# Kernel optimization log

Hardware: AMD Instinct MI355X
Metric: run time of the kernel (lower is better)

## Reference

```python
import jax, jax.numpy as jnp
import numpy as np

B, H, W = 64, 256, 256
G = 64
V = G * G          # 4096
HID = 512
S = 50


def _conv(x, w, b):
    # x: (B,C,H,W), w: (O,I,3,3) -> 'same' conv, NCHW
    y = jax.lax.conv_general_dilated(x, w, (1, 1), 'SAME',
                                     dimension_numbers=('NCHW', 'OIHW', 'NCHW'))
    return y + b[None, :, None, None]


def setup_inputs() -> dict:
    key = jax.random.key(0)
    ks = jax.random.split(key, 14)

    def lin(k, shape, fan_in):
        return (jax.random.normal(k, shape, jnp.float32) / np.float32(np.sqrt(fan_in)))

    return {
        'mask': jax.random.uniform(ks[0], (B, 1, H, W), jnp.float32),
        'target_ids': jax.random.randint(ks[1], (B, S), 0, V),
        'conv1_w': lin(ks[2], (16, 1, 3, 3), 9), 'conv1_b': jnp.zeros((16,), jnp.float32),
        'conv2_w': lin(ks[3], (32, 16, 3, 3), 16 * 9), 'conv2_b': jnp.zeros((32,), jnp.float32),
        'feat_w': lin(ks[4], (HID, 32), 32), 'feat_b': jnp.zeros((HID,), jnp.float32),
        'ctx_w': lin(ks[5], (HID, HID), HID), 'ctx_b': jnp.zeros((HID,), jnp.float32),
        'tok_emb': jax.random.normal(ks[6], (V + 1, HID), jnp.float32) * 0.02,
        'w_ih': lin(ks[7], (4 * HID, HID), HID), 'w_hh': lin(ks[8], (4 * HID, HID), HID),
        'b_ih': jnp.zeros((4 * HID,), jnp.float32), 'b_hh': jnp.zeros((4 * HID,), jnp.float32),
        'head_w': lin(ks[9], (V, HID), HID), 'head_b': jnp.zeros((V,), jnp.float32),
    }


def reference(mask, target_ids, conv1_w, conv1_b, conv2_w, conv2_b,
              feat_w, feat_b, ctx_w, ctx_b, tok_emb,
              w_ih, w_hh, b_ih, b_hh, head_w, head_b):
    b = mask.shape[0]
    vocab = head_w.shape[0]

    # --- CNN encoder ---
    x = jax.nn.relu(_conv(mask, conv1_w, conv1_b))                    # (B,16,H,W)
    x = jax.lax.reduce_window(x, -jnp.inf, jax.lax.max,
                              (1, 1, 2, 2), (1, 1, 2, 2), 'VALID')    # (B,16,H/2,W/2)
    x = jax.nn.relu(_conv(x, conv2_w, conv2_b))                       # (B,32,H/2,W/2)
    x = x.mean(axis=(2, 3))                                           # AdaptiveAvgPool2d(1) -> (B,32)

    h0 = x @ feat_w.T + feat_b                                        # (B,HID)
    c0 = jnp.zeros_like(h0)
    ctx = h0 @ ctx_w.T + ctx_b                                        # (B,HID)

    # Full teacher forcing (ratio=1.0): input token at t=0 is start token V,
    # at t>0 it is target_ids[:, t-1]. All embeddings gathered upfront.
    start = jnp.full((b, 1), vocab, dtype=target_ids.dtype)
    toks = jnp.concatenate([start, target_ids[:, :-1]], axis=1)       # (B,S)
    embs = tok_emb[toks]                                              # (B,S,HID)
    lstm_in = jnp.swapaxes(embs, 0, 1) + ctx[None]                    # (S,B,HID)

    bias = b_ih + b_hh

    def step(carry, inp):
        h, c = carry
        gates = inp @ w_ih.T + h @ w_hh.T + bias                      # (B,4*HID)
        i, f, g, o = jnp.split(gates, 4, axis=-1)
        c = jax.nn.sigmoid(f) * c + jax.nn.sigmoid(i) * jnp.tanh(g)
        h = jax.nn.sigmoid(o) * jnp.tanh(c)
        logit = h @ head_w.T + head_b                                 # (B,V)
        return (h, c), logit

    _, logits = jax.lax.scan(step, (h0, c0), lstm_in)                 # (S,B,V)
    return jnp.swapaxes(logits, 0, 1)                                 # (B,S,V)
```

## Files before the change

### kernel.cpp

```cpp
#include <hip/hip_runtime.h>
#include <cmath>

typedef __attribute__((ext_vector_type(8))) _Float16 f16x8;
typedef __attribute__((ext_vector_type(4))) float f32x4;
typedef __attribute__((ext_vector_type(4))) unsigned u32x4;

#define LSTM_NB 32

__device__ __forceinline__ unsigned short f2h(float x) {
  return __builtin_bit_cast(unsigned short, (_Float16)x);
}

__device__ __forceinline__ void gload16(const void* g, void* l) {
  __builtin_amdgcn_global_load_lds(
      (const __attribute__((address_space(1))) void*)g,
      (__attribute__((address_space(3))) void*)l, 16, 0, 0);
}

__device__ __forceinline__ void cload16(const void* p, u32x4* dst) {
  asm volatile("global_load_dwordx4 %0, %1, off sc0 sc1"
               : "=v"(*dst)
               : "v"(p));
}

__global__ __launch_bounds__(512) void k_conv(
    const float* __restrict__ mask, const float* __restrict__ w1,
    const float* __restrict__ b1, const float* __restrict__ w2,
    const float* __restrict__ b2, float* __restrict__ part)
{
  __shared__ float s_p1[16][18 * 36];
  __shared__ float s_w1[144];
  __shared__ float s_b1[16];
  __shared__ float s_w2[4608];
  __shared__ float s_b2[32];

  const int tid = threadIdx.x;
  const int b = blockIdx.x >> 5;
  const int tile = blockIdx.x & 31;
  const int px0 = (tile & 3) * 32, py0 = (tile >> 2) * 16;
  const float* mb = mask + (size_t)b * 65536;

  for (int i = tid; i < 144; i += 512) s_w1[i] = w1[i];
  for (int i = tid; i < 4608; i += 512) s_w2[i] = w2[i];
  if (tid < 16) s_b1[tid] = b1[tid];
  if (tid < 32) s_b2[tid] = b2[tid];
  __syncthreads();

  for (int idx = tid; idx < 18 * 34; idx += 512) {
    int ly = idx / 34, lx = idx - ly * 34;
    int py = py0 - 1 + ly, px = px0 - 1 + lx;
    if (py < 0 || py >= 128 || px < 0 || px >= 128) {
      for (int o = 0; o < 16; o++) s_p1[o][ly * 36 + lx] = 0.f;
    } else {
      float patch[4][4];
      int gy0 = 2 * py - 1, gx0 = 2 * px - 1;
#pragma unroll
      for (int i = 0; i < 4; i++) {
        int gy = gy0 + i;
        bool yok = (gy >= 0 && gy < 256);
#pragma unroll
        for (int j = 0; j < 4; j++) {
          int gx = gx0 + j;
          patch[i][j] = (yok && gx >= 0 && gx < 256) ? mb[gy * 256 + gx] : 0.f;
        }
      }
      for (int o = 0; o < 16; o++) {
        float m = 0.f;
#pragma unroll
        for (int dy = 0; dy < 2; dy++)
#pragma unroll
          for (int dx = 0; dx < 2; dx++) {
            float v = s_b1[o];
#pragma unroll
            for (int ky = 0; ky < 3; ky++)
#pragma unroll
              for (int kx = 0; kx < 3; kx++)
                v = fmaf(patch[dy + ky][dx + kx], s_w1[o * 9 + ky * 3 + kx], v);
            m = fmaxf(m, v);
          }
        s_p1[o][ly * 36 + lx] = m;
      }
    }
  }
  __syncthreads();

  const int ocg = tid >> 6;
  const int sp = tid & 63;
  const int sx = (sp & 7) * 4, sy = (sp >> 3) * 2;
  float acc[4][8];
#pragma unroll
  for (int a = 0; a < 4; a++)
#pragma unroll
    for (int q = 0; q < 8; q++) acc[a][q] = 0.f;

  for (int ic = 0; ic < 16; ic++) {
    float p[4][6];
#pragma unroll
    for (int i = 0; i < 4; i++) {
      const float* row = &s_p1[ic][(sy + i) * 36 + sx];
#pragma unroll
      for (int j = 0; j < 6; j++) p[i][j] = row[j];
    }
#pragma unroll
    for (int o4 = 0; o4 < 4; o4++) {
      const int oc = ocg * 4 + o4;
      const float* w = &s_w2[(oc * 16 + ic) * 9];
      float w00 = w[0], w01 = w[1], w02 = w[2];
      float w10 = w[3], w11 = w[4], w12 = w[5];
      float w20 = w[6], w21 = w[7], w22 = w[8];
#pragma unroll
      for (int y = 0; y < 2; y++)
#pragma unroll
        for (int x = 0; x < 4; x++) {
          float s = acc[o4][y * 4 + x];
          s = fmaf(p[y][x], w00, s);
          s = fmaf(p[y][x + 1], w01, s);
          s = fmaf(p[y][x + 2], w02, s);
          s = fmaf(p[y + 1][x], w10, s);
          s = fmaf(p[y + 1][x + 1], w11, s);
          s = fmaf(p[y + 1][x + 2], w12, s);
          s = fmaf(p[y + 2][x], w20, s);
          s = fmaf(p[y + 2][x + 1], w21, s);
          s = fmaf(p[y + 2][x + 2], w22, s);
          acc[o4][y * 4 + x] = s;
        }
    }
  }

  const int lane = tid & 63;
#pragma unroll
  for (int o4 = 0; o4 < 4; o4++) {
    float bv = s_b2[ocg * 4 + o4];
    float s = 0.f;
#pragma unroll
    for (int q = 0; q < 8; q++) s += fmaxf(acc[o4][q] + bv, 0.f);
    for (int off = 32; off > 0; off >>= 1) s += __shfl_down(s, off, 64);
    if (lane == 0) part[(b * 32 + tile) * 32 + ocg * 4 + o4] = s;
  }
}

__global__ __launch_bounds__(256) void k_pool_h0(
    const float* __restrict__ part, const float* __restrict__ feat_w,
    const float* __restrict__ feat_b, float* __restrict__ h0,
    unsigned short* __restrict__ h0f)
{
  const int b = blockIdx.x, tid = threadIdx.x;
  __shared__ float pl[32];
  if (tid < 32) {
    float s = 0.f;
    for (int t = 0; t < 32; t++) s += part[(b * 32 + t) * 32 + tid];
    pl[tid] = s * (1.0f / 16384.0f);
  }
  __syncthreads();
  for (int j = tid; j < 512; j += 256) {
    float acc = feat_b[j];
    const float* w = feat_w + j * 32;
#pragma unroll
    for (int ic = 0; ic < 32; ic++) acc = fmaf(pl[ic], w[ic], acc);
    h0[b * 512 + j] = acc;
    h0f[b * 512 + j] = f2h(acc);
  }
}

__global__ __launch_bounds__(256) void k_ctx(
    const float* __restrict__ h0, const float* __restrict__ ctx_w,
    const float* __restrict__ ctx_b, float* __restrict__ ctx)
{
  const int b = blockIdx.x, tid = threadIdx.x;
  __shared__ float hs[512];
  for (int k = tid; k < 512; k += 256) hs[k] = h0[b * 512 + k];
  __syncthreads();
  for (int j = tid; j < 512; j += 256) {
    const float* w = ctx_w + (size_t)j * 512;
    float s0 = 0.f, s1 = 0.f, s2 = 0.f, s3 = 0.f;
    for (int k = 0; k < 512; k += 4) {
      float4 w4 = *(const float4*)(w + k);
      s0 = fmaf(hs[k], w4.x, s0);
      s1 = fmaf(hs[k + 1], w4.y, s1);
      s2 = fmaf(hs[k + 2], w4.z, s2);
      s3 = fmaf(hs[k + 3], w4.w, s3);
    }
    ctx[b * 512 + j] = ctx_b[j] + ((s0 + s1) + (s2 + s3));
  }
}

__global__ __launch_bounds__(256) void k_f2h(
    const float* __restrict__ in, unsigned short* __restrict__ out, int n)
{
  int i = (blockIdx.x * 256 + threadIdx.x) * 4;
  if (i < n) {
    float4 v = *(const float4*)(in + i);
    unsigned lo = (unsigned)f2h(v.x) | ((unsigned)f2h(v.y) << 16);
    unsigned hi = (unsigned)f2h(v.z) | ((unsigned)f2h(v.w) << 16);
    *(uint2*)(out + i) = make_uint2(lo, hi);
  }
}

__global__ __launch_bounds__(64) void k_zero(int* __restrict__ p) {
  p[threadIdx.x] = 0;
}
__global__ __launch_bounds__(256) void k_zero_f(float* __restrict__ p) {
  p[blockIdx.x * 256 + threadIdx.x] = 0.f;
}

__global__ __launch_bounds__(128) void k_build_A(
    const float* __restrict__ tok_emb, const int* __restrict__ tgt,
    const float* __restrict__ ctx, unsigned short* __restrict__ A)
{
  const int r = blockIdx.x;
  const int t = r >> 6, b = r & 63;
  const int tok = (t == 0) ? 4096 : tgt[b * 50 + (t - 1)];
  const int i = threadIdx.x * 4;
  float4 ev = *(const float4*)(tok_emb + (size_t)tok * 512 + i);
  float4 cv = *(const float4*)(ctx + b * 512 + i);
  unsigned lo = (unsigned)f2h(ev.x + cv.x) | ((unsigned)f2h(ev.y + cv.y) << 16);
  unsigned hi = (unsigned)f2h(ev.z + cv.z) | ((unsigned)f2h(ev.w + cv.w) << 16);
  *(uint2*)(A + (size_t)r * 512 + i) = make_uint2(lo, hi);
}

template <int MODE>
__global__ __launch_bounds__(256) void k_gemm_mfma(
    const unsigned short* __restrict__ A, const unsigned short* __restrict__ B,
    const float* __restrict__ bias_a, const float* __restrict__ bias_b,
    float* __restrict__ C, int NB)
{
  __shared__ unsigned short sA[128 * 32];
  __shared__ unsigned short sB[128 * 32];
  const int tid = threadIdx.x;
  const int bx = blockIdx.x % NB, by = blockIdx.x / NB;
  const int lane = tid & 63, wv = tid >> 6;
  const int wr = wv >> 1, wc = wv & 1;
  const unsigned short* Ab = A + (size_t)by * 128 * 512;
  const unsigned short* Bb = B + (size_t)bx * 128 * 512;

  f32x4 acc[4][4];
#pragma unroll
  for (int m = 0; m < 4; m++)
#pragma unroll
    for (int n = 0; n < 4; n++) acc[m][n] = (f32x4){0.f, 0.f, 0.f, 0.f};

  const int r0 = tid >> 2, c0 = (tid & 3) * 8;
  const int idx1 = tid + 256;
  const int r1 = idx1 >> 2, c1 = (idx1 & 3) * 8;
  unsigned short* lA0 = sA + (size_t)wv * 512;
  unsigned short* lA1 = sA + 2048 + (size_t)wv * 512;
  unsigned short* lB0 = sB + (size_t)wv * 512;
  unsigned short* lB1 = sB + 2048 + (size_t)wv * 512;

  const int frow = lane & 15;
  const int foff = (lane >> 4) * 8;

  for (int kc = 0; kc < 512; kc += 32) {
    gload16(Ab + (size_t)r0 * 512 + kc + c0, lA0);
    gload16(Ab + (size_t)r1 * 512 + kc + c1, lA1);
    gload16(Bb + (size_t)r0 * 512 + kc + c0, lB0);
    gload16(Bb + (size_t)r1 * 512 + kc + c1, lB1);
    __syncthreads();

    f16x8 af[4], bfr[4];
#pragma unroll
    for (int m = 0; m < 4; m++)
      af[m] = *(const f16x8*)(sA + (wr * 64 + m * 16 + frow) * 32 + foff);
#pragma unroll
    for (int n = 0; n < 4; n++)
      bfr[n] = *(const f16x8*)(sB + (wc * 64 + n * 16 + frow) * 32 + foff);
#pragma unroll
    for (int m = 0; m < 4; m++)
#pragma unroll
      for (int n = 0; n < 4; n++)
        acc[m][n] = __builtin_amdgcn_mfma_f32_16x16x32_f16(
            af[m], bfr[n], acc[m][n], 0, 0, 0);
    __syncthreads();
  }

#pragma unroll
  for (int n = 0; n < 4; n++) {
    const int gc = bx * 128 + wc * 64 + n * 16 + (lane & 15);
    const float bv = (MODE == 0) ? (bias_a[gc] + bias_b[gc]) : bias_a[gc];
#pragma unroll
    for (int m = 0; m < 4; m++) {
      const int rb = by * 128 + wr * 64 + m * 16 + (lane >> 4) * 4;
#pragma unroll
      for (int j = 0; j < 4; j++) {
        const int r = rb + j;
        float v = acc[m][n][j] + bv;
        int t = r >> 6, bb = r & 63;
        if (MODE == 0) {
          C[(size_t)t * 131072 + (size_t)gc * 64 + bb] = v;
        } else {
          C[((size_t)bb * 50 + t) * 4096 + gc] = v;
        }
      }
    }
  }
}

__global__ __launch_bounds__(256, 1) void k_lstm_mfma(
    const float* __restrict__ xgT,
    const float* __restrict__ w_hh,
    const unsigned short* __restrict__ h0f,
    unsigned short* __restrict__ hallf,
    int* __restrict__ cnt)
{
  __shared__ unsigned short s_h[64 * 512];
  __shared__ float s_g[4][64][17];
  const int tid = threadIdx.x;
  const int kb = blockIdx.x;
  const int g = tid >> 6;
  const int lane = tid & 63;
  const int frow = lane & 15;
  const int foff = (lane >> 4) * 8;

  f16x8 wf[16];
  {
    const float* wrow = w_hh + (size_t)(g * 512 + kb * 16 + frow) * 512;
#pragma unroll
    for (int kf = 0; kf < 16; kf++) {
      float tmp[8];
      *(float4*)tmp = *(const float4*)(wrow + kf * 32 + foff);
      *(float4*)(tmp + 4) = *(const float4*)(wrow + kf * 32 + foff + 4);
#pragma unroll
      for (int j = 0; j < 8; j++) wf[kf][j] = (_Float16)tmp[j];
    }
  }

  float c[4] = {0.f, 0.f, 0.f, 0.f};
  const int b2 = tid & 63, dd2 = tid >> 6;

  for (int t = 0; t < 50; ++t) {
    const unsigned short* H = t ? hallf + (size_t)(t - 1) * 32768 : h0f;

    const float* xr =
        xgT + (size_t)t * 131072 + (size_t)(kb * 16 + dd2 * 4) * 64 + b2;
    float xv[16];
#pragma unroll
    for (int gq = 0; gq < 4; gq++)
#pragma unroll
      for (int i = 0; i < 4; i++)
        xv[gq * 4 + i] = xr[(size_t)(gq * 512 + i) * 64];

    {
      u32x4 r[16];
#pragma unroll
      for (int i = 0; i < 16; i++)
        cload16((const char*)H + (size_t)(tid + i * 256) * 16, &r[i]);
      asm volatile("s_waitcnt vmcnt(0)" ::: "memory");
      __builtin_amdgcn_sched_barrier(0);
#pragma unroll
      for (int i = 0; i < 16; i++) {
        int byte = (tid + i * 256) * 16;
        int swz = byte ^ (((byte >> 10) & 7) << 4);
        *(u32x4*)((char*)s_h + swz) = r[i];
      }
    }
    __syncthreads();

    f32x4 acc[4];
#pragma unroll
    for (int mt = 0; mt < 4; mt++) acc[mt] = (f32x4){0.f, 0.f, 0.f, 0.f};
#pragma unroll
    for (int kf = 0; kf < 16; kf++) {
#pragma unroll
      for (int mt = 0; mt < 4; mt++) {
        const int row = mt * 16 + frow;
        const int byte = (row << 10) + kf * 64 + foff * 2;
        const int swz = byte ^ ((row & 7) << 4);
        f16x8 ah = *(const f16x8*)((const char*)s_h + swz);
        acc[mt] =
            __builtin_amdgcn_mfma_f32_16x16x32_f16(ah, wf[kf], acc[mt], 0, 0, 0);
      }
    }
#pragma unroll
    for (int mt = 0; mt < 4; mt++)
#pragma unroll
      for (int j = 0; j < 4; j++)
        s_g[g][mt * 16 + (lane >> 4) * 4 + j][frow] = acc[mt][j];
    __syncthreads();

    unsigned long long qf = 0;
#pragma unroll
    for (int i = 0; i < 4; i++) {
      float gi = s_g[0][b2][dd2 * 4 + i] + xv[0 + i];
      float gf = s_g[1][b2][dd2 * 4 + i] + xv[4 + i];
      float gg = s_g[2][b2][dd2 * 4 + i] + xv[8 + i];
      float go = s_g[3][b2][dd2 * 4 + i] + xv[12 + i];
      float ig = 1.f / (1.f + expf(-gi));
      float fg = 1.f / (1.f + expf(-gf));
      float og = 1.f / (1.f + expf(-go));
      float gt = tanhf(gg);
      c[i] = fmaf(fg, c[i], ig * gt);
      float h = og * tanhf(c[i]);
      qf |= (unsigned long long)f2h(h) << (16 * i);
    }
    const size_t ho = (size_t)b2 * 512 + kb * 16 + dd2 * 4;
    __hip_atomic_store((unsigned long long*)(hallf + (size_t)t * 32768 + ho),
                       qf, __ATOMIC_RELAXED, __HIP_MEMORY_SCOPE_AGENT);
    __syncthreads();
    if (tid == 0) {
      __hip_atomic_fetch_add(&cnt[t], 1, __ATOMIC_RELAXED,
                             __HIP_MEMORY_SCOPE_AGENT);
      while (__hip_atomic_load(&cnt[t], __ATOMIC_RELAXED,
                               __HIP_MEMORY_SCOPE_AGENT) < LSTM_NB) {
        __builtin_amdgcn_s_sleep(1);
      }
    }
    __syncthreads();
  }
}

__global__ __launch_bounds__(256) void k_lstm_step1(
    const float* __restrict__ xgT, const float* __restrict__ w_hh,
    const float* __restrict__ hin, float* __restrict__ hout,
    unsigned short* __restrict__ hallf_t, float* __restrict__ cbuf, int t)
{
  __shared__ float s_w[8][512];
  __shared__ float s_g[2][4][64];
  const int tid = threadIdx.x;
  const int dd0 = blockIdx.x * 2;

  for (int idx = tid; idx < 1024; idx += 256) {
    int row = idx >> 7;
    int k4 = (idx & 127) << 2;
    int q_ = row >> 1, dd_i = row & 1;
    *(float4*)&s_w[row][k4] =
        *(const float4*)(w_hh + (size_t)(q_ * 512 + dd0 + dd_i) * 512 + k4);
  }
  const int b = tid & 63;
  const int q = tid >> 6;
  __syncthreads();

  const float* hc = hin + b * 512;
  const float* xr = xgT + (size_t)t * 131072 + (size_t)(q * 512 + dd0) * 64 + b;
  float a0 = xr[0], a1 = xr[64];
  const float* w0 = s_w[q * 2 + 0];
  const float* w1 = s_w[q * 2 + 1];
#pragma unroll 8
  for (int k = 0; k < 512; k += 4) {
    float4 h4 = *(const float4*)(hc + k);
    float4 u = *(const float4*)(w0 + k);
    float4 v = *(const float4*)(w1 + k);
    a0 = fmaf(h4.x, u.x, fmaf(h4.y, u.y, fmaf(h4.z, u.z, fmaf(h4.w, u.w, a0))));
    a1 = fmaf(h4.x, v.x, fmaf(h4.y, v.y, fmaf(h4.z, v.z, fmaf(h4.w, v.w, a1))));
  }
  s_g[0][q][b] = a0;
  s_g[1][q][b] = a1;
  __syncthreads();
  if (q < 2) {
    const int dd = dd0 + q;
    float gi = s_g[q][0][b], gf = s_g[q][1][b];
    float gg = s_g[q][2][b], go = s_g[q][3][b];
    float ig = 1.f / (1.f + expf(-gi));
    float fg = 1.f / (1.f + expf(-gf));
    float og = 1.f / (1.f + expf(-go));
    float gt = tanhf(gg);
    float c = fmaf(fg, cbuf[b * 512 + dd], ig * gt);
    float h = og * tanhf(c);
    cbuf[b * 512 + dd] = c;
    hout[b * 512 + dd] = h;
    hallf_t[(size_t)b * 512 + dd] = f2h(h);
  }
}

extern "C" void kernel_launch(void* const* d_in, const int* in_sizes, int n_in,
                              void* d_out, int out_size, void* d_ws,
                              size_t ws_size, hipStream_t stream) {
  const float* mask   = (const float*)d_in[0];
  const int*   tgt    = (const int*)d_in[1];
  const float* w1     = (const float*)d_in[2];
  const float* b1     = (const float*)d_in[3];
  const float* w2     = (const float*)d_in[4];
  const float* b2     = (const float*)d_in[5];
  const float* feat_w = (const float*)d_in[6];
  const float* feat_b = (const float*)d_in[7];
  const float* ctx_w  = (const float*)d_in[8];
  const float* ctx_b  = (const float*)d_in[9];
  const float* temb   = (const float*)d_in[10];
  const float* w_ih   = (const float*)d_in[11];
  const float* w_hh_p = (const float*)d_in[12];
  const float* b_ih   = (const float*)d_in[13];
  const float* b_hh   = (const float*)d_in[14];
  const float* head_w = (const float*)d_in[15];
  const float* head_b = (const float*)d_in[16];

  float* ws = (float*)d_ws;
  float* part  = ws;
  float* hbuf  = ws + 65536;
  float* ctx   = ws + 131072;
  int*   cnt   = (int*)(ws + 163840);
  unsigned short* h0f  = (unsigned short*)(ws + 163904);
  unsigned short* Ab16 = (unsigned short*)(ws + 180288);
  unsigned short* hallf = Ab16;
  unsigned short* wihb = (unsigned short*)(ws + 999488);
  unsigned short* hwb  = (unsigned short*)(ws + 1523776);
  float* xgT   = ws + 2572352;
  float* cbuf  = part;
  float* out   = (float*)d_out;

  k_conv<<<2048, 512, 0, stream>>>(mask, w1, b1, w2, b2, part);
  k_f2h<<<1024, 256, 0, stream>>>(w_ih, wihb, 1048576);
  k_f2h<<<2048, 256, 0, stream>>>(head_w, hwb, 2097152);
  k_zero<<<1, 64, 0, stream>>>(cnt);
  k_pool_h0<<<64, 256, 0, stream>>>(part, feat_w, feat_b, hbuf, h0f);
  k_ctx<<<64, 256, 0, stream>>>(hbuf, ctx_w, ctx_b, ctx);
  k_build_A<<<3200, 128, 0, stream>>>(temb, tgt, ctx, Ab16);
  k_gemm_mfma<0><<<25 * 16, 256, 0, stream>>>(Ab16, wihb, b_ih, b_hh, xgT, 16);

  {
    const float* xgT_c = xgT;
    const float* whh_c = w_hh_p;
    const unsigned short* h0f_c = h0f;
    unsigned short* hallf_c = hallf;
    int* cnt_c = cnt;
    void* args[] = {(void*)&xgT_c, (void*)&whh_c, (void*)&h0f_c,
                    (void*)&hallf_c, (void*)&cnt_c};
    hipError_t e = hipLaunchCooperativeKernel(
        (const void*)k_lstm_mfma, dim3(LSTM_NB), dim3(256), args, 0, stream);
    if (e != hipSuccess) {
      (void)hipGetLastError();
      k_zero_f<<<128, 256, 0, stream>>>(cbuf);
      for (int t = 0; t < 50; t++) {
        const float* hin = hbuf + (t & 1) * 32768;
        float* hout = hbuf + ((t + 1) & 1) * 32768;
        k_lstm_step1<<<256, 256, 0, stream>>>(
            xgT, w_hh_p, hin, hout, hallf + (size_t)t * 32768, cbuf, t);
      }
    }
  }

  k_gemm_mfma<1><<<25 * 32, 256, 0, stream>>>(hallf, hwb, head_b, nullptr, out, 32);
}
```

Measured before the change: 568.3 us.

## Store pooled conv1 activations as fp16 in LDS and fuse small prep kernels

The pooled conv1 tile in shared memory is now stored as fp16 instead of fp32. This halves LDS footprint, which may allow more blocks per CU, and halves LDS read traffic in conv2. The pool/feat and ctx kernels are merged into one, and the two weight fp16 conversions plus the counter zeroing are merged into one prep kernel, cutting launch count. The fp16 intermediate adds rounding error to the conv2 input.

```diff
diff --git a/kernel.cpp b/kernel.cpp
--- a/kernel.cpp
+++ b/kernel.cpp
@@ -9,6 +9,11 @@
 
 __device__ __forceinline__ unsigned short f2h(float x) {
   return __builtin_bit_cast(unsigned short, (_Float16)x);
+}
+
+__device__ __forceinline__ void h2f2(unsigned u, float& a, float& b) {
+  a = (float)__builtin_bit_cast(_Float16, (unsigned short)(u & 0xffffu));
+  b = (float)__builtin_bit_cast(_Float16, (unsigned short)(u >> 16));
 }
 
 __device__ __forceinline__ void gload16(const void* g, void* l) {
@@ -28,7 +33,7 @@
     const float* __restrict__ b1, const float* __restrict__ w2,
     const float* __restrict__ b2, float* __restrict__ part)
 {
-  __shared__ float s_p1[16][18 * 36];
+  __shared__ unsigned short s_p1[16][18 * 36];
   __shared__ float s_w1[144];
   __shared__ float s_b1[16];
   __shared__ float s_w2[4608];
@@ -50,7 +55,7 @@
     int ly = idx / 34, lx = idx - ly * 34;
     int py = py0 - 1 + ly, px = px0 - 1 + lx;
     if (py < 0 || py >= 128 || px < 0 || px >= 128) {
-      for (int o = 0; o < 16; o++) s_p1[o][ly * 36 + lx] = 0.f;
+      for (int o = 0; o < 16; o++) s_p1[o][ly * 36 + lx] = 0;
     } else {
       float patch[4][4];
       int gy0 = 2 * py - 1, gx0 = 2 * px - 1;
@@ -78,7 +83,7 @@
                 v = fmaf(patch[dy + ky][dx + kx], s_w1[o * 9 + ky * 3 + kx], v);
             m = fmaxf(m, v);
           }
-        s_p1[o][ly * 36 + lx] = m;
+        s_p1[o][ly * 36 + lx] = f2h(m);
       }
     }
   }
@@ -97,9 +102,13 @@
     float p[4][6];
 #pragma unroll
     for (int i = 0; i < 4; i++) {
-      const float* row = &s_p1[ic][(sy + i) * 36 + sx];
-#pragma unroll
-      for (int j = 0; j < 6; j++) p[i][j] = row[j];
+      const unsigned short* row = &s_p1[ic][(sy + i) * 36 + sx];
+      unsigned u0 = *(const unsigned*)(row);
+      unsigned u1 = *(const unsigned*)(row + 2);
+      unsigned u2 = *(const unsigned*)(row + 4);
+      h2f2(u0, p[i][0], p[i][1]);
+      h2f2(u1, p[i][2], p[i][3]);
+      h2f2(u2, p[i][4], p[i][5]);
     }
 #pragma unroll
     for (int o4 = 0; o4 < 4; o4++) {
@@ -139,13 +148,15 @@
   }
 }
 
-__global__ __launch_bounds__(256) void k_pool_h0(
+__global__ __launch_bounds__(256) void k_pool_ctx(
     const float* __restrict__ part, const float* __restrict__ feat_w,
-    const float* __restrict__ feat_b, float* __restrict__ h0,
-    unsigned short* __restrict__ h0f)
+    const float* __restrict__ feat_b, const float* __restrict__ ctx_w,
+    const float* __restrict__ ctx_b, float* __restrict__ h0,
+    unsigned short* __restrict__ h0f, float* __restrict__ ctx)
 {
   const int b = blockIdx.x, tid = threadIdx.x;
   __shared__ float pl[32];
+  __shared__ float hs[512];
   if (tid < 32) {
     float s = 0.f;
     for (int t = 0; t < 32; t++) s += part[(b * 32 + t) * 32 + tid];
@@ -159,16 +170,8 @@
     for (int ic = 0; ic < 32; ic++) acc = fmaf(pl[ic], w[ic], acc);
     h0[b * 512 + j] = acc;
     h0f[b * 512 + j] = f2h(acc);
-  }
-}
-
-__global__ __launch_bounds__(256) void k_ctx(
-    const float* __restrict__ h0, const float* __restrict__ ctx_w,
-    const float* __restrict__ ctx_b, float* __restrict__ ctx)
-{
-  const int b = blockIdx.x, tid = threadIdx.x;
-  __shared__ float hs[512];
-  for (int k = tid; k < 512; k += 256) hs[k] = h0[b * 512 + k];
+    hs[j] = acc;
+  }
   __syncthreads();
   for (int j = tid; j < 512; j += 256) {
     const float* w = ctx_w + (size_t)j * 512;
@@ -184,21 +187,27 @@
   }
 }
 
-__global__ __launch_bounds__(256) void k_f2h(
-    const float* __restrict__ in, unsigned short* __restrict__ out, int n)
-{
-  int i = (blockIdx.x * 256 + threadIdx.x) * 4;
-  if (i < n) {
-    float4 v = *(const float4*)(in + i);
+__global__ __launch_bounds__(256) void k_prep(
+    const float* __restrict__ wih, const float* __restrict__ hw,
+    unsigned short* __restrict__ wihb, unsigned short* __restrict__ hwb,
+    int* __restrict__ cnt)
+{
+  const int i = blockIdx.x * 256 + threadIdx.x;
+  if (i < 64) cnt[i] = 0;
+  if (i < 262144) {
+    float4 v = *(const float4*)(wih + (size_t)i * 4);
     unsigned lo = (unsigned)f2h(v.x) | ((unsigned)f2h(v.y) << 16);
     unsigned hi = (unsigned)f2h(v.z) | ((unsigned)f2h(v.w) << 16);
-    *(uint2*)(out + i) = make_uint2(lo, hi);
-  }
-}
-
-__global__ __launch_bounds__(64) void k_zero(int* __restrict__ p) {
-  p[threadIdx.x] = 0;
-}
+    *(uint2*)(wihb + (size_t)i * 4) = make_uint2(lo, hi);
+  } else if (i < 786432) {
+    const int j = i - 262144;
+    float4 v = *(const float4*)(hw + (size_t)j * 4);
+    unsigned lo = (unsigned)f2h(v.x) | ((unsigned)f2h(v.y) << 16);
+    unsigned hi = (unsigned)f2h(v.z) | ((unsigned)f2h(v.w) << 16);
+    *(uint2*)(hwb + (size_t)j * 4) = make_uint2(lo, hi);
+  }
+}
+
 __global__ __launch_bounds__(256) void k_zero_f(float* __restrict__ p) {
   p[blockIdx.x * 256 + threadIdx.x] = 0.f;
 }
@@ -497,11 +506,9 @@
   float* out   = (float*)d_out;
 
   k_conv<<<2048, 512, 0, stream>>>(mask, w1, b1, w2, b2, part);
-  k_f2h<<<1024, 256, 0, stream>>>(w_ih, wihb, 1048576);
-  k_f2h<<<2048, 256, 0, stream>>>(head_w, hwb, 2097152);
-  k_zero<<<1, 64, 0, stream>>>(cnt);
-  k_pool_h0<<<64, 256, 0, stream>>>(part, feat_w, feat_b, hbuf, h0f);
-  k_ctx<<<64, 256, 0, stream>>>(hbuf, ctx_w, ctx_b, ctx);
+  k_prep<<<3072, 256, 0, stream>>>(w_ih, head_w, wihb, hwb, cnt);
+  k_pool_ctx<<<64, 256, 0, stream>>>(part, feat_w, feat_b, ctx_w, ctx_b,
+                                     hbuf, h0f, ctx);
   k_build_A<<<3200, 128, 0, stream>>>(temb, tgt, ctx, Ab16);
   k_gemm_mfma<0><<<25 * 16, 256, 0, stream>>>(Ab16, wihb, b_ih, b_hh, xgT, 16);
 
```

Result: faster. 545.2 us (-4.1%).
